# Kernel optimization log

Measured on AMD Instinct MI355X. Metric: run time of the kernel, lower is better.

The kernel has to match this reference:

```python
import jax, jax.numpy as jnp
import numpy as np

GROUPS = [1, 2, 2, 3]

def setup_inputs() -> dict:
    key = jax.random.key(0)
    ks = jax.random.split(key, 8)
    b, dim, h, w = 8, 256, 64, 64
    return {
        "x": jax.random.normal(ks[0], (b, dim, h, w), dtype=jnp.float32),
        "temperature": jnp.ones((4, 1, 1), dtype=jnp.float32),          # nn.Parameter(torch.ones(4,1,1))
        "w_qkv": jax.random.normal(ks[1], (3 * dim, dim)) * 0.02,        # Conv2d(dim,3dim,1,bias=False)
        "w_dw": jax.random.normal(ks[2], (3 * dim, 1, 3, 3)) * 0.1,      # depthwise 3x3, groups=3dim
        "w_proj": jax.random.normal(ks[3], (dim, dim)) * 0.02,           # Conv2d(dim,dim,1,bias=False)
        "w_gate": jax.random.normal(ks[4], (dim, dim)) * 0.02,           # Intra gatingConv (Conv1d k=1)
        "b_gate": jnp.zeros((dim,), dtype=jnp.float32),
        "w_down": jax.random.normal(ks[5], (dim // 2, dim)) * 0.02,      # Intra down
        "b_down": jnp.zeros((dim // 2,), dtype=jnp.float32),
        "w_up": jax.random.normal(ks[6], (dim, dim // 2)) * 0.02,        # Intra up
        "b_up": jnp.zeros((dim,), dtype=jnp.float32),
    }

def _l2norm(t):
    # torch F.normalize(dim=-1): x / max(||x||, 1e-12)
    return t / jnp.maximum(jnp.linalg.norm(t, axis=-1, keepdims=True), 1e-12)

def reference(x, temperature, w_qkv, w_dw, w_proj, w_gate, b_gate, w_down, b_down, w_up, b_up):
    b, c, h, w = x.shape
    L = h * w
    # qkv = dwconv3x3(conv1x1(x))
    qkv = jnp.einsum('bchw,oc->bohw', x, w_qkv)
    qkv = jax.lax.conv_general_dilated(qkv, w_dw, (1, 1), ((1, 1), (1, 1)),
                                       feature_group_count=3 * c,
                                       dimension_numbers=('NCHW', 'OIHW', 'NCHW'))
    q, k, v = jnp.split(qkv, 3, axis=1)
    q = q.reshape(b, c, L); k = k.reshape(b, c, L); v = v.reshape(b, c, L)
    # ReGroup: sort channels by mean activation (descending), split per ratio
    order = jnp.argsort(-q.mean(axis=2).mean(axis=0))
    qs, ks_, vs = q[:, order], k[:, order], v[:, order]
    total = sum(GROUPS)
    sizes = [int(r / total * c) for r in GROUPS]
    sizes[-1] += c - sum(sizes)
    outs, caches = [], []
    start = 0
    for i, g in enumerate(sizes):
        qg = qs[:, start:start + g]; kg = ks_[:, start:start + g]; vg = vs[:, start:start + g]
        start += g
        qn = _l2norm(qg); kn = _l2norm(kg)
        attn = jax.nn.softmax(jnp.einsum('bcl,bdl->bcd', qn, kn) * temperature[i], axis=-1)  # (b,Cg,Cg)
        caches.append(jax.lax.stop_gradient(qn + kn))  # q.detach()+k.detach()
        outs.append(jnp.einsum('bcd,bdl->bcl', attn, vg))
    # CalculateCurrentLayerCache: mean over L, channel-tile to c, bilinear 1x1->sxs == broadcast
    s = int(L ** 0.5 + 0.9999)
    accum = jnp.zeros((b, c), dtype=x.dtype)
    for tc, g in zip(caches, sizes):
        gm = tc.mean(axis=-1)                     # (b, Cg)
        rep = max(1, c // g)
        tiled = jnp.tile(gm, (1, rep))
        if tiled.shape[1] > c:
            tiled = tiled[:, :c]
        elif tiled.shape[1] < c:
            tiled = jnp.pad(tiled, ((0, 0), (0, c - tiled.shape[1])))
        accum = accum + tiled
    accum = accum / len(caches)
    qv_cache = 0.9 * jnp.broadcast_to(accum[:, :, None, None], (b, c, s, s))
    out_all = jnp.concatenate(outs, axis=1)       # (b, c, L)
    tmp_caches = jnp.concatenate(caches, axis=1)  # (b, c, L)
    # Intra_CacheModulation: gated = gelu(gateConv(z)) * z ; out = up(down(gated))
    z = tmp_caches + out_all
    gating = jax.nn.gelu(jnp.einsum('oc,bcl->bol', w_gate, z) + b_gate[None, :, None], approximate=False)
    gated = gating * z
    mid = jnp.einsum('oc,bcl->bol', w_down, gated) + b_down[None, :, None]
    intra = jnp.einsum('oc,bcl->bol', w_up, mid) + b_up[None, :, None]
    out_all = (intra + out_all).reshape(b, c, h, w)
    out_all = jnp.einsum('bchw,oc->bohw', out_all, w_proj)
    return (out_all, qv_cache)
```

## Files before the change

kernel.cpp:

```cpp
#include <hip/hip_runtime.h>
#include <hip/hip_fp16.h>
#include <math.h>

#define B 8
#define C 256
#define L 4096
#define OC3 768

typedef __attribute__((ext_vector_type(8))) short short8v;
typedef __attribute__((ext_vector_type(8))) unsigned short u16x8;
typedef __attribute__((ext_vector_type(4))) float f32x4;

__device__ __forceinline__ float gelu_exact(float x){
  return 0.5f * x * (1.0f + erff(x * 0.70710678118654752440f));
}
__device__ __forceinline__ float wave_sum(float v){
  #pragma unroll
  for (int off = 32; off > 0; off >>= 1) v += __shfl_down(v, off, 64);
  return v;
}
__device__ __forceinline__ unsigned short f16b(float f){
  return __half_as_ushort(__float2half_rn(f));
}
__device__ __forceinline__ float f16tof(unsigned short u){
  return __half2float(__ushort_as_half(u));
}
__device__ __forceinline__ unsigned int splitpackh(float v){
  unsigned short hi = f16b(v);
  float lof = v - f16tof(hi);
  unsigned short lo = f16b(lof);
  return (unsigned int)hi | ((unsigned int)lo << 16);
}
__device__ __forceinline__ void gl16(const unsigned short* g, unsigned short* l){
  __builtin_amdgcn_global_load_lds(
      (const __attribute__((address_space(1))) void*)g,
      (__attribute__((address_space(3))) void*)l, 16, 0, 0);
}

__global__ __launch_bounds__(256) void wsplit_kernel(
    const float* __restrict__ wqkv, const float* __restrict__ wgate,
    const float* __restrict__ wdown, const float* __restrict__ wup,
    const float* __restrict__ wproj,
    unsigned short* __restrict__ Wf16,
    unsigned short* __restrict__ PH, unsigned short* __restrict__ PLo)
{
  int idx = blockIdx.x * 256 + threadIdx.x;
  if (idx < 327680) {
    float s;
    if (idx < 196608)      s = wqkv[idx];
    else if (idx < 262144) s = wgate[idx - 196608];
    else if (idx < 294912) s = wdown[idx - 262144];
    else                   s = wup[idx - 294912];
    Wf16[idx] = f16b(s);
  } else {
    int j = idx - 327680;
    float wv = wproj[j];
    unsigned short hh = f16b(wv);
    PH[j]  = hh;
    PLo[j] = f16b(wv - f16tof(hh));
  }
}

__global__ __launch_bounds__(256) void splitx_kernel(const float* __restrict__ x,
    unsigned short* __restrict__ XThi, unsigned short* __restrict__ XTlo)
{
  __shared__ float st[64][68];
  const int b = blockIdx.z, c0 = blockIdx.y * 64, lb = blockIdx.x * 64;
  const int t = threadIdx.x;
  #pragma unroll
  for (int i = 0; i < 4; i++) {
    int row = (t >> 4) + i * 16;
    int col = (t & 15) * 4;
    float4 v = *(const float4*)&x[((size_t)b * C + c0 + row) * L + lb + col];
    st[row][col] = v.x; st[row][col+1] = v.y; st[row][col+2] = v.z; st[row][col+3] = v.w;
  }
  __syncthreads();
  const int l = t >> 2, cq = t & 3;
  u16x8 hv0, hv1, lv0, lv1;
  #pragma unroll
  for (int i = 0; i < 16; i++) {
    unsigned int p = splitpackh(st[cq * 16 + i][l]);
    if (i < 8) { hv0[i] = (unsigned short)(p & 0xFFFFu); lv0[i] = (unsigned short)(p >> 16); }
    else       { hv1[i-8] = (unsigned short)(p & 0xFFFFu); lv1[i-8] = (unsigned short)(p >> 16); }
  }
  size_t o = ((size_t)b * L + lb + l) * C + c0 + cq * 16;
  *(u16x8*)&XThi[o]     = hv0;
  *(u16x8*)&XThi[o + 8] = hv1;
  *(u16x8*)&XTlo[o]     = lv0;
  *(u16x8*)&XTlo[o + 8] = lv1;
}

template<int KTOT, int EPI, int MODE>
__global__ __launch_bounds__(256) void hgemm(
    const unsigned short* __restrict__ Ahi_g, const unsigned short* __restrict__ Alo_g,
    const unsigned short* __restrict__ Bw_g,
    float* __restrict__ outF,
    unsigned short* __restrict__ outH,
    int Ntot)
{
  __shared__ unsigned short SB[2][3][128 * 32];
  const int t  = threadIdx.x;
  const int lb = blockIdx.x * 128;
  const int o0 = blockIdx.y * 128;
  const int b  = blockIdx.z;
  const int w  = t >> 6, lane = t & 63;
  const int wm = w >> 1, wn = w & 1;
  const int ln = lane & 15, lg = lane >> 4;
  const int lrow  = lane >> 2;
  const int chunk = (lane & 3) ^ ((lane >> 4) & 3);
  const int slot  = lg ^ (ln >> 2);
  const bool twop = (blockIdx.y < 2);

  f32x4 z4 = {0.f, 0.f, 0.f, 0.f};
  f32x4 acc[4][4];
  #pragma unroll
  for (int i = 0; i < 4; i++)
    #pragma unroll
    for (int j = 0; j < 4; j++) acc[i][j] = z4;

  const size_t arow0 = (size_t)b * L + lb;
  constexpr int NKT = KTOT / 32;

  auto stage = [&](int kt, int cb) {
    const int k0 = kt * 32;
    #pragma unroll
    for (int i = 0; i < 2; i++) {
      const int rb = w * 32 + i * 16;
      const size_t ga = (arow0 + rb + lrow) * KTOT + k0 + chunk * 8;
      gl16(Ahi_g + ga, &SB[cb][0][rb * 32]);
      if (twop) gl16(Alo_g + ga, &SB[cb][1][rb * 32]);
      const size_t gb = (size_t)(o0 + rb + lrow) * KTOT + k0 + chunk * 8;
      gl16(Bw_g + gb, &SB[cb][2][rb * 32]);
    }
  };

  stage(0, 0);
  __syncthreads();
  int cur = 0;
  for (int kt = 0; kt < NKT; ++kt) {
    if (kt + 1 < NKT) stage(kt + 1, cur ^ 1);
    short8v bwf[4];
    #pragma unroll
    for (int nf = 0; nf < 4; nf++) {
      const int off = (wn * 64 + nf * 16 + ln) * 32 + slot * 8;
      bwf[nf] = *(const short8v*)&SB[cur][2][off];
    }
    #pragma unroll
    for (int mf = 0; mf < 4; mf++) {
      const int off = (wm * 64 + mf * 16 + ln) * 32 + slot * 8;
      const short8v ah = *(const short8v*)&SB[cur][0][off];
      #pragma unroll
      for (int nf = 0; nf < 4; nf++)
        acc[mf][nf] = __builtin_amdgcn_mfma_f32_16x16x32_f16(ah, bwf[nf], acc[mf][nf], 0, 0, 0);
      if (twop) {
        const short8v al = *(const short8v*)&SB[cur][1][off];
        #pragma unroll
        for (int nf = 0; nf < 4; nf++)
          acc[mf][nf] = __builtin_amdgcn_mfma_f32_16x16x32_f16(al, bwf[nf], acc[mf][nf], 0, 0, 0);
      }
    }
    __syncthreads();
    cur ^= 1;
  }
  #pragma unroll
  for (int mf = 0; mf < 4; mf++) {
    const int mbase = lb + wm * 64 + mf * 16 + lg * 4;
    #pragma unroll
    for (int nf = 0; nf < 4; nf++) {
      const int o = o0 + wn * 64 + nf * 16 + ln;
      if (o0 < 256) {
        float4 r;
        r.x = acc[mf][nf][0]; r.y = acc[mf][nf][1];
        r.z = acc[mf][nf][2]; r.w = acc[mf][nf][3];
        *(float4*)&outF[((size_t)b * 256 + o) * L + mbase] = r;
      } else {
        ushort4 r;
        r.x = f16b(acc[mf][nf][0]); r.y = f16b(acc[mf][nf][1]);
        r.z = f16b(acc[mf][nf][2]); r.w = f16b(acc[mf][nf][3]);
        *(ushort4*)&outH[((size_t)b * 512 + (o - 256)) * L + mbase] = r;
      }
    }
  }
}

__global__ __launch_bounds__(256, 2) void mlp_fused_kernel(
    const unsigned short* __restrict__ zT,
    const unsigned short* __restrict__ outT,
    const unsigned short* __restrict__ Wg,
    const unsigned short* __restrict__ Wd,
    const unsigned short* __restrict__ Wu,
    const unsigned short* __restrict__ WpH,
    const unsigned short* __restrict__ WpL,
    const float* __restrict__ bg, const float* __restrict__ bd, const float* __restrict__ bu,
    float* __restrict__ out0)
{
  __shared__ unsigned short zL[64 * 256];
  __shared__ unsigned short wL[2][64 * 128];
  __shared__ unsigned short mL[64 * 128];
  const int t = threadIdx.x;
  const int l0 = blockIdx.x * 64;
  const int b  = blockIdx.y;
  const int w = t >> 6, lane = t & 63;
  const int ln = lane & 15, lg = lane >> 4;

  {
    const int rIn = lane >> 5, ch = lane & 31;
    #pragma unroll
    for (int j = 0; j < 8; j++) {
      const int rowbase = w * 16 + j * 2;
      const int row = rowbase + rIn;
      const int sc = ch ^ (row & 7);
      gl16(zT + ((size_t)b * L + l0 + row) * 256 + sc * 8, &zL[rowbase * 256]);
    }
  }
  auto issueW = [&](int cb, const unsigned short* src, int rowstride) {
    const int rIn = lane >> 4, ch = lane & 15;
    #pragma unroll
    for (int j = 0; j < 4; j++) {
      const int rowbase = j * 16 + w * 4;
      const int row = rowbase + rIn;
      const int sc = ch ^ (row & 7);
      gl16(src + (size_t)row * rowstride + sc * 8, &wL[cb][rowbase * 128]);
    }
  };
  auto fragZ = [&](int row, int cc) -> short8v {
    return *(const short8v*)&zL[row * 256 + (cc ^ (row & 7)) * 8];
  };
  auto fragW = [&](int cb, int row, int cc) -> short8v {
    return *(const short8v*)&wL[cb][row * 128 + (cc ^ (row & 7)) * 8];
  };
  auto fragM = [&](int row, int cc) -> short8v {
    return *(const short8v*)&mL[row * 128 + (cc ^ (row & 7)) * 8];
  };
  auto gemmZt = [&](f32x4 (&acc)[4], int buf, int cbase) {
    #pragma unroll
    for (int ks = 0; ks < 4; ks++) {
      const short8v af = fragZ(w * 16 + ln, cbase + ks * 4 + lg);
      #pragma unroll
      for (int nf = 0; nf < 4; nf++) {
        const short8v bf = fragW(buf, nf * 16 + ln, ks * 4 + lg);
        acc[nf] = __builtin_amdgcn_mfma_f32_16x16x32_f16(af, bf, acc[nf], 0, 0, 0);
      }
    }
  };
  auto gemmMt = [&](f32x4 (&acc)[4], int buf) {
    #pragma unroll
    for (int ks = 0; ks < 4; ks++) {
      const short8v af = fragM(w * 16 + ln, ks * 4 + lg);
      #pragma unroll
      for (int nf = 0; nf < 4; nf++) {
        const short8v bf = fragW(buf, nf * 16 + ln, ks * 4 + lg);
        acc[nf] = __builtin_amdgcn_mfma_f32_16x16x32_f16(af, bf, acc[nf], 0, 0, 0);
      }
    }
  };

  const f32x4 zz = {0.f, 0.f, 0.f, 0.f};
  issueW(0, Wg, 256);
  __syncthreads();

  f32x4 aG[4][4];
  #pragma unroll
  for (int i = 0; i < 4; i++)
    #pragma unroll
    for (int j = 0; j < 4; j++) aG[i][j] = zz;
  issueW(1, Wg + 128,           256); gemmZt(aG[0], 0, 0);  __syncthreads();
  issueW(0, Wg + 64*256,        256); gemmZt(aG[0], 1, 16); __syncthreads();
  issueW(1, Wg + 64*256 + 128,  256); gemmZt(aG[1], 0, 0);  __syncthreads();
  issueW(0, Wg + 128*256,       256); gemmZt(aG[1], 1, 16); __syncthreads();
  issueW(1, Wg + 128*256 + 128, 256); gemmZt(aG[2], 0, 0);  __syncthreads();
  issueW(0, Wg + 192*256,       256); gemmZt(aG[2], 1, 16); __syncthreads();
  issueW(1, Wg + 192*256 + 128, 256); gemmZt(aG[3], 0, 0);  __syncthreads();
  issueW(0, Wd,                 256); gemmZt(aG[3], 1, 16); __syncthreads();
  #pragma unroll
  for (int oc = 0; oc < 4; oc++)
    #pragma unroll
    for (int nf = 0; nf < 4; nf++)
      #pragma unroll
      for (int r = 0; r < 4; r++) {
        const int l = w * 16 + lg * 4 + r;
        const int o = oc * 64 + nf * 16 + ln;
        const int a = l * 256 + (((o >> 3) ^ (l & 7)) << 3) + (o & 7);
        zL[a] = f16b(gelu_exact(aG[oc][nf][r] + bg[o]) * f16tof(zL[a]));
      }
  f32x4 aD[2][4];
  #pragma unroll
  for (int i = 0; i < 2; i++)
    #pragma unroll
    for (int j = 0; j < 4; j++) aD[i][j] = zz;
  issueW(1, Wd + 128,           256); gemmZt(aD[0], 0, 0);  __syncthreads();
  issueW(0, Wd + 64*256,        256); gemmZt(aD[0], 1, 16); __syncthreads();
  issueW(1, Wd + 64*256 + 128,  256); gemmZt(aD[1], 0, 0);  __syncthreads();
  issueW(0, Wu,                 128); gemmZt(aD[1], 1, 16); __syncthreads();
  #pragma unroll
  for (int oc = 0; oc < 2; oc++)
    #pragma unroll
    for (int nf = 0; nf < 4; nf++)
      #pragma unroll
      for (int r = 0; r < 4; r++) {
        const int l = w * 16 + lg * 4 + r;
        const int o = oc * 64 + nf * 16 + ln;
        mL[l * 128 + (((o >> 3) ^ (l & 7)) << 3) + (o & 7)] = f16b(aD[oc][nf][r] + bd[o]);
      }
  f32x4 aU[4][4];
  #pragma unroll
  for (int i = 0; i < 4; i++)
    #pragma unroll
    for (int j = 0; j < 4; j++) aU[i][j] = zz;
  issueW(1, Wu + 64*128,        128); gemmMt(aU[0], 0); __syncthreads();
  issueW(0, Wu + 128*128,       128); gemmMt(aU[1], 1); __syncthreads();
  issueW(1, Wu + 192*128,       128); gemmMt(aU[2], 0); __syncthreads();
  issueW(0, WpH,                256); gemmMt(aU[3], 1); __syncthreads();
  #pragma unroll
  for (int oc = 0; oc < 4; oc++)
    #pragma unroll
    for (int nf = 0; nf < 4; nf++)
      #pragma unroll
      for (int r = 0; r < 4; r++) {
        const int l = w * 16 + lg * 4 + r;
        const int o = oc * 64 + nf * 16 + ln;
        const float v = aU[oc][nf][r] + bu[o]
                      + f16tof(outT[((size_t)b * L + l0 + l) * 256 + o]);
        zL[l * 256 + (((o >> 3) ^ (l & 7)) << 3) + (o & 7)] = f16b(v);
      }
  f32x4 aP[4][4];
  #pragma unroll
  for (int i = 0; i < 4; i++)
    #pragma unroll
    for (int j = 0; j < 4; j++) aP[i][j] = zz;
  issueW(1, WpL,                256); gemmZt(aP[0], 0, 0);  __syncthreads();
  issueW(0, WpH + 128,          256); gemmZt(aP[0], 1, 0);  __syncthreads();
  issueW(1, WpL + 128,          256); gemmZt(aP[0], 0, 16); __syncthreads();
  issueW(0, WpH + 64*256,       256); gemmZt(aP[0], 1, 16); __syncthreads();
  issueW(1, WpL + 64*256,       256); gemmZt(aP[1], 0, 0);  __syncthreads();
  issueW(0, WpH + 64*256 + 128, 256); gemmZt(aP[1], 1, 0);  __syncthreads();
  issueW(1, WpL + 64*256 + 128, 256); gemmZt(aP[1], 0, 16); __syncthreads();
  issueW(0, WpH + 128*256,      256); gemmZt(aP[1], 1, 16); __syncthreads();
  issueW(1, WpL + 128*256,      256); gemmZt(aP[2], 0, 0);  __syncthreads();
  issueW(0, WpH + 128*256 + 128,256); gemmZt(aP[2], 1, 0);  __syncthreads();
  issueW(1, WpL + 128*256 + 128,256); gemmZt(aP[2], 0, 16); __syncthreads();
  issueW(0, WpH + 192*256,      256); gemmZt(aP[2], 1, 16); __syncthreads();
  issueW(1, WpL + 192*256,      256); gemmZt(aP[3], 0, 0);  __syncthreads();
  issueW(0, WpH + 192*256 + 128,256); gemmZt(aP[3], 1, 0);  __syncthreads();
  issueW(1, WpL + 192*256 + 128,256); gemmZt(aP[3], 0, 16); __syncthreads();
                                      gemmZt(aP[3], 1, 16);
  #pragma unroll
  for (int oc = 0; oc < 4; oc++)
    #pragma unroll
    for (int nf = 0; nf < 4; nf++) {
      const int o = oc * 64 + nf * 16 + ln;
      float4 r4;
      r4.x = aP[oc][nf][0]; r4.y = aP[oc][nf][1];
      r4.z = aP[oc][nf][2]; r4.w = aP[oc][nf][3];
      *(float4*)&out0[((size_t)b * 256 + o) * L + l0 + w * 16 + lg * 4] = r4;
    }
}

__global__ __launch_bounds__(256) void dwconv2_kernel(
    const float* __restrict__ inQ, const unsigned short* __restrict__ inKV,
    const float* __restrict__ wdw,
    unsigned short* __restrict__ qkF, unsigned short* __restrict__ vF,
    float* __restrict__ csum, float* __restrict__ csumsq)
{
  __shared__ float p[66][73];
  __shared__ float rs[4][2];
  const int ch = blockIdx.x;
  const int b  = blockIdx.y;
  const int t  = threadIdx.x;
  float wt[9];
  #pragma unroll
  for (int j = 0; j < 9; j++) wt[j] = wdw[ch * 9 + j];
  if (t < 66) { p[0][3 + t] = 0.f; p[65][3 + t] = 0.f; }
  if (t < 64) { p[1 + t][3] = 0.f; p[1 + t][68] = 0.f; }
  if (ch < 256) {
    const size_t base = ((size_t)b * 256 + ch) * L;
    #pragma unroll
    for (int i = 0; i < 4; i++) {
      int pix = (i * 256 + t) * 4;
      const float4 v = *reinterpret_cast<const float4*>(&inQ[base + pix]);
      int h = pix >> 6, ww = pix & 63;
      p[1+h][4+ww] = v.x; p[1+h][5+ww] = v.y; p[1+h][6+ww] = v.z; p[1+h][7+ww] = v.w;
    }
  } else {
    const size_t base = ((size_t)b * 512 + (ch - 256)) * L + t * 16;
    const u16x8 a0 = *(const u16x8*)&inKV[base];
    const u16x8 a1 = *(const u16x8*)&inKV[base + 8];
    const int h = t >> 2, w0 = (t & 3) * 16;
    #pragma unroll
    for (int j = 0; j < 8; j++) {
      p[1+h][4+w0+j]   = f16tof((unsigned short)a0[j]);
      p[1+h][12+w0+j]  = f16tof((unsigned short)a1[j]);
    }
  }
  __syncthreads();
  const int h  = t >> 2;
  const int w0 = (t & 3) * 16;
  float r0a[18], r1a[18], r2a[18];
  #pragma unroll
  for (int c = 0; c < 18; c++) {
    r0a[c] = p[h][w0 + 3 + c];
    r1a[c] = p[h + 1][w0 + 3 + c];
    r2a[c] = p[h + 2][w0 + 3 + c];
  }
  float res[16];
  float s = 0.f, s2 = 0.f;
  #pragma unroll
  for (int j = 0; j < 16; j++) {
    float acc;
    acc = r0a[j] * wt[0];
    acc = fmaf(r0a[j+1], wt[1], acc);
    acc = fmaf(r0a[j+2], wt[2], acc);
    acc = fmaf(r1a[j],   wt[3], acc);
    acc = fmaf(r1a[j+1], wt[4], acc);
    acc = fmaf(r1a[j+2], wt[5], acc);
    acc = fmaf(r2a[j],   wt[6], acc);
    acc = fmaf(r2a[j+1], wt[7], acc);
    acc = fmaf(r2a[j+2], wt[8], acc);
    res[j] = acc;
    s += acc;
    s2 = fmaf(acc, acc, s2);
  }
  u16x8 h0v, h1v;
  #pragma unroll
  for (int j = 0; j < 16; j++) {
    if (j < 8) h0v[j]   = f16b(res[j]);
    else       h1v[j-8] = f16b(res[j]);
  }
  if (ch < 512) {
    const size_t qi = ((size_t)b * 512 + ch) * L + t * 16;
    *(u16x8*)&qkF[qi]     = h0v;
    *(u16x8*)&qkF[qi + 8] = h1v;
    s = wave_sum(s); s2 = wave_sum(s2);
    const int lane = t & 63, wid = t >> 6;
    if (lane == 0) { rs[wid][0] = s; rs[wid][1] = s2; }
    __syncthreads();
    if (t == 0) {
      csum[b * 512 + ch]   = rs[0][0] + rs[1][0] + rs[2][0] + rs[3][0];
      csumsq[b * 512 + ch] = rs[0][1] + rs[1][1] + rs[2][1] + rs[3][1];
    }
  } else {
    const size_t vi = ((size_t)b * 256 + (ch - 512)) * L + t * 16;
    *(u16x8*)&vF[vi]     = h0v;
    *(u16x8*)&vF[vi + 8] = h1v;
  }
}

__global__ __launch_bounds__(256) void rankstats_kernel(
    const float* __restrict__ csum, const float* __restrict__ csumsq,
    int* __restrict__ order,
    float* __restrict__ sumq, float* __restrict__ sumk,
    float* __restrict__ invnq, float* __restrict__ invnk)
{
  const int c = threadIdx.x;
  float key = 0.f;
  #pragma unroll
  for (int b = 0; b < 8; b++) key += csum[b * 512 + c];
  __shared__ float keys[256];
  __shared__ int ordS[256];
  keys[c] = key;
  __syncthreads();
  int rank = 0;
  for (int j = 0; j < 256; j++) {
    float kj = keys[j];
    rank += (kj > key) || (kj == key && j < c);
  }
  order[rank] = c;
  ordS[rank] = c;
  __syncthreads();
  const int ch = ordS[c];
  #pragma unroll
  for (int b = 0; b < 8; b++) {
    sumq[b * 256 + c]  = csum[b * 512 + ch];
    invnq[b * 256 + c] = 1.0f / fmaxf(sqrtf(csumsq[b * 512 + ch]), 1e-12f);
    sumk[b * 256 + c]  = csum[b * 512 + 256 + ch];
    invnk[b * 256 + c] = 1.0f / fmaxf(sqrtf(csumsq[b * 512 + 256 + ch]), 1e-12f);
  }
}

__global__ __launch_bounds__(256) void vpack_kernel(
    const unsigned short* __restrict__ vF, const unsigned short* __restrict__ qkF,
    const int* __restrict__ order,
    const float* __restrict__ invnq, const float* __restrict__ invnk,
    unsigned short* __restrict__ vTS, unsigned short* __restrict__ zqT)
{
  __shared__ float vt[64][65];
  __shared__ float zt[64][65];
  __shared__ int   ordS[256];
  __shared__ float iqS[256], ikS[256];
  const int t = threadIdx.x, lb = blockIdx.x * 64, b = blockIdx.y;
  ordS[t] = order[t];
  iqS[t] = invnq[b * 256 + t];
  ikS[t] = invnk[b * 256 + t];
  __syncthreads();
  for (int cc = 0; cc < 4; cc++) {
    const int r0 = cc * 64;
    for (int i = t; i < 1024; i += 256) {
      const int row = i >> 4, q = i & 15;
      const int ch = ordS[r0 + row];
      const float iq = iqS[r0 + row], ik = ikS[r0 + row];
      const ushort4 v4 = *(const ushort4*)&vF[((size_t)b * 256 + ch) * L + lb + q * 4];
      vt[q*4+0][row] = f16tof(v4.x); vt[q*4+1][row] = f16tof(v4.y);
      vt[q*4+2][row] = f16tof(v4.z); vt[q*4+3][row] = f16tof(v4.w);
      const ushort4 q4 = *(const ushort4*)&qkF[((size_t)b * 512 + ch) * L + lb + q * 4];
      const ushort4 k4 = *(const ushort4*)&qkF[((size_t)b * 512 + 256 + ch) * L + lb + q * 4];
      zt[q*4+0][row] = f16tof(q4.x) * iq + f16tof(k4.x) * ik;
      zt[q*4+1][row] = f16tof(q4.y) * iq + f16tof(k4.y) * ik;
      zt[q*4+2][row] = f16tof(q4.z) * iq + f16tof(k4.z) * ik;
      zt[q*4+3][row] = f16tof(q4.w) * iq + f16tof(k4.w) * ik;
    }
    __syncthreads();
    const int l = t >> 2, qq = t & 3;
    const size_t ob = ((size_t)b * L + lb + l) * 256 + r0 + qq * 16;
    u16x8 vv[2], zz[2];
    #pragma unroll
    for (int j = 0; j < 16; j++) {
      vv[j>>3][j&7] = f16b(vt[l][qq*16 + j]);
      zz[j>>3][j&7] = f16b(zt[l][qq*16 + j]);
    }
    *(u16x8*)&vTS[ob]     = vv[0]; *(u16x8*)&vTS[ob + 8] = vv[1];
    *(u16x8*)&zqT[ob]     = zz[0]; *(u16x8*)&zqT[ob + 8] = zz[1];
    __syncthreads();
  }
}

template<int G, int GI, int START, int MB, int SPB>
__device__ void scores_body(const unsigned short* __restrict__ qkF,
    const int* __restrict__ order, float* __restrict__ Spart,
    unsigned short* Ah, unsigned short* Bh, int* ordS)
{
  constexpr int MR = (G - MB * 64 < 64) ? (G - MB * 64) : 64;
  constexpr int NF = G / 16;
  const int t = threadIdx.x, ks = blockIdx.x, b = blockIdx.y;
  const int w = t >> 6, lane = t & 63, ln = lane & 15, lg = lane >> 4;
  const int lrow  = lane >> 2;
  const int chunk = (lane & 3) ^ ((lane >> 4) & 3);
  const int slot  = lg ^ (ln >> 2);
  for (int i = t; i < G; i += 256) ordS[i] = order[START + i];
  __syncthreads();
  const int k0 = ks * 512;
  const bool act = (w * 16) < MR;
  f32x4 z4 = {0.f, 0.f, 0.f, 0.f};
  f32x4 acc[NF];
  #pragma unroll
  for (int i = 0; i < NF; i++) acc[i] = z4;

  auto stage = [&](int kc, int cb) {
    for (int i = w; i < MR / 16; i += 4) {
      const int rb = i * 16;
      const int ch = ordS[MB * 64 + rb + lrow];
      const size_t g = ((size_t)b * 512 + ch) * L + k0 + kc + chunk * 8;
      gl16(qkF + g, &Ah[cb * 2048 + rb * 32]);
    }
    for (int i = w; i < G / 16; i += 4) {
      const int rb = i * 16;
      const int ch = 256 + ordS[rb + lrow];
      const size_t g = ((size_t)b * 512 + ch) * L + k0 + kc + chunk * 8;
      gl16(qkF + g, &Bh[cb * 3072 + rb * 32]);
    }
  };

  stage(0, 0);
  __syncthreads();
  int cur = 0;
  for (int kc = 0; kc < 512; kc += 32) {
    if (kc + 32 < 512) stage(kc + 32, cur ^ 1);
    if (act) {
      const int aoff = cur * 2048 + (w * 16 + ln) * 32 + slot * 8;
      const short8v ah = *(const short8v*)&Ah[aoff];
      #pragma unroll
      for (int nf = 0; nf < NF; nf++) {
        const int boff = cur * 3072 + (nf * 16 + ln) * 32 + slot * 8;
        const short8v bh = *(const short8v*)&Bh[boff];
        acc[nf] = __builtin_amdgcn_mfma_f32_16x16x32_f16(ah, bh, acc[nf], 0, 0, 0);
      }
    }
    __syncthreads();
    cur ^= 1;
  }
  if (act) {
    float* dst = Spart + (size_t)b * 147456 + SPB + ks * G * G;
    #pragma unroll
    for (int nf = 0; nf < NF; nf++) {
      const int d = nf * 16 + ln;
      #pragma unroll
      for (int r = 0; r < 4; r++) {
        const int m = MB * 64 + w * 16 + lg * 4 + r;
        dst[m * G + d] = acc[nf][r];
      }
    }
  }
}

__global__ __launch_bounds__(256) void scores_kernel(const unsigned short* __restrict__ qkF,
    const int* __restrict__ order, float* __restrict__ Spart)
{
  __shared__ unsigned short Ah[2 * 64 * 32];
  __shared__ unsigned short Bh[2 * 96 * 32];
  __shared__ int ordS[96];
  switch (blockIdx.z) {
    case 0:  scores_body<32, 0, 0,   0, 0    >(qkF, order, Spart, Ah, Bh, ordS); break;
    case 1:  scores_body<64, 1, 32,  0, 8192 >(qkF, order, Spart, Ah, Bh, ordS); break;
    case 2:  scores_body<64, 2, 96,  0, 40960>(qkF, order, Spart, Ah, Bh, ordS); break;
    case 3:  scores_body<96, 3, 160, 0, 73728>(qkF, order, Spart, Ah, Bh, ordS); break;
    default: scores_body<96, 3, 160, 1, 73728>(qkF, order, Spart, Ah, Bh, ordS); break;
  }
}

template<int G, int GI, int START, int SPB, int AOFF>
__device__ void softmax_body(const float* __restrict__ Spart, const float* __restrict__ invnq,
    const float* __restrict__ invnk, const float* __restrict__ temperature,
    unsigned short* __restrict__ attnP, float* Sm)
{
  constexpr int RQ = G / 4;
  const int t = threadIdx.x;
  const int b = blockIdx.x;
  const int r0 = blockIdx.z * RQ;
  const float temp = temperature[GI];
  for (int idx = t; idx < RQ * G; idx += 256) {
    const int rl = idx / G, d = idx - rl * G;
    const int gidx = (r0 + rl) * G + d;
    float s = 0.f;
    #pragma unroll
    for (int ks = 0; ks < 8; ks++)
      s += Spart[(size_t)b * 147456 + SPB + ks * G * G + gidx];
    Sm[idx] = s * invnq[b * 256 + START + r0 + rl] * invnk[b * 256 + START + d] * temp;
  }
  __syncthreads();
  const int wv = t >> 6, lane = t & 63;
  for (int r = wv; r < RQ; r += 4) {
    const float v0 = (lane < G) ? Sm[r * G + lane] : -INFINITY;
    const float v1 = (64 + lane < G) ? Sm[r * G + 64 + lane] : -INFINITY;
    float m = fmaxf(v0, v1);
    #pragma unroll
    for (int off = 32; off > 0; off >>= 1) m = fmaxf(m, __shfl_xor(m, off, 64));
    const float e0 = (lane < G) ? expf(v0 - m) : 0.f;
    const float e1 = (64 + lane < G) ? expf(v1 - m) : 0.f;
    float s = e0 + e1;
    #pragma unroll
    for (int off = 32; off > 0; off >>= 1) s += __shfl_xor(s, off, 64);
    const float inv = 1.0f / s;
    const size_t base = (size_t)b * 18432 + AOFF + (size_t)(r0 + r) * G;
    if (lane < G)      attnP[base + lane]      = f16b(e0 * inv);
    if (64 + lane < G) attnP[base + 64 + lane] = f16b(e1 * inv);
  }
}

__global__ __launch_bounds__(256) void softmax_kernel(const float* __restrict__ Spart,
    const float* __restrict__ invnq, const float* __restrict__ invnk,
    const float* __restrict__ temperature, unsigned short* __restrict__ attnP)
{
  extern __shared__ float smem[];
  switch (blockIdx.y) {
    case 0:  softmax_body<32, 0, 0,   0,     0   >(Spart, invnq, invnk, temperature, attnP, smem); break;
    case 1:  softmax_body<64, 1, 32,  8192,  1024>(Spart, invnq, invnk, temperature, attnP, smem); break;
    case 2:  softmax_body<64, 2, 96,  40960, 5120>(Spart, invnq, invnk, temperature, attnP, smem); break;
    default: softmax_body<96, 3, 160, 73728, 9216>(Spart, invnq, invnk, temperature, attnP, smem); break;
  }
}

template<int G, int GI, int START, int AOFF>
__device__ void pv_body(
    const unsigned short* __restrict__ vTS, const unsigned short* __restrict__ attnP,
    const unsigned short* __restrict__ zqT,
    unsigned short* __restrict__ outT, unsigned short* __restrict__ zT,
    unsigned short* Ah, unsigned short* Bh)
{
  constexpr int NF = G / 16;
  const int t = threadIdx.x, b = blockIdx.y, l0 = blockIdx.x * 128;
  const int w = t >> 6, lane = t & 63, ln = lane & 15, lg = lane >> 4;
  const int lrow  = lane >> 2;
  const int chunk = (lane & 3) ^ ((lane >> 4) & 3);
  const int slot  = lg ^ (ln >> 2);
  f32x4 z4 = {0.f, 0.f, 0.f, 0.f};
  f32x4 acc[2][NF];
  #pragma unroll
  for (int i = 0; i < 2; i++)
    #pragma unroll
    for (int j = 0; j < NF; j++) acc[i][j] = z4;
  for (int kc = 0; kc < G; kc += 32) {
    #pragma unroll
    for (int i = 0; i < 2; i++) {
      const int rb = w * 32 + i * 16;
      const size_t g = ((size_t)b * L + l0 + rb + lrow) * 256 + START + kc + chunk * 8;
      gl16(vTS + g, &Ah[rb * 32]);
    }
    for (int i = w; i < G / 16; i += 4) {
      const int rb = i * 16;
      const size_t g = (size_t)b * 18432 + AOFF + (size_t)(rb + lrow) * G + kc + chunk * 8;
      gl16(attnP + g, &Bh[rb * 32]);
    }
    __syncthreads();
    short8v bhf[NF];
    #pragma unroll
    for (int nf = 0; nf < NF; nf++)
      bhf[nf] = *(const short8v*)&Bh[(nf * 16 + ln) * 32 + slot * 8];
    #pragma unroll
    for (int mi = 0; mi < 2; mi++) {
      const int aoff = ((w * 2 + mi) * 16 + ln) * 32 + slot * 8;
      const short8v ah = *(const short8v*)&Ah[aoff];
      #pragma unroll
      for (int nf = 0; nf < NF; nf++)
        acc[mi][nf] = __builtin_amdgcn_mfma_f32_16x16x32_f16(ah, bhf[nf], acc[mi][nf], 0, 0, 0);
    }
    __syncthreads();
  }
  #pragma unroll
  for (int mi = 0; mi < 2; mi++) {
    const int lbase = l0 + (w * 2 + mi) * 16 + lg * 4;
    #pragma unroll
    for (int nf = 0; nf < NF; nf++) {
      const int col = START + nf * 16 + ln;
      #pragma unroll
      for (int r = 0; r < 4; r++) {
        const size_t idx = ((size_t)b * L + lbase + r) * 256 + col;
        const float v = acc[mi][nf][r];
        outT[idx] = f16b(v);
        zT[idx]   = f16b(v + f16tof(zqT[idx]));
      }
    }
  }
}

__global__ __launch_bounds__(256) void pv_kernel(
    const unsigned short* __restrict__ vTS, const unsigned short* __restrict__ attnP,
    const unsigned short* __restrict__ zqT,
    unsigned short* __restrict__ outT, unsigned short* __restrict__ zT)
{
  __shared__ unsigned short Ah[128 * 32];
  __shared__ unsigned short Bh[96 * 32];
  switch (blockIdx.z) {
    case 0:  pv_body<32, 0, 0,   0   >(vTS, attnP, zqT, outT, zT, Ah, Bh); break;
    case 1:  pv_body<64, 1, 32,  1024>(vTS, attnP, zqT, outT, zT, Ah, Bh); break;
    case 2:  pv_body<64, 2, 96,  5120>(vTS, attnP, zqT, outT, zT, Ah, Bh); break;
    default: pv_body<96, 3, 160, 9216>(vTS, attnP, zqT, outT, zT, Ah, Bh); break;
  }
}

__global__ __launch_bounds__(256) void qv_kernel(const float* __restrict__ sumq,
    const float* __restrict__ sumk, const float* __restrict__ invnq,
    const float* __restrict__ invnk, float* __restrict__ out2)
{
  const int b = blockIdx.x >> 8, r = blockIdx.x & 255;
  float val = 0.f;
  {
    const int idx = b * 256 + 0 + (r & 31);
    val += fmaf(sumq[idx], invnq[idx], sumk[idx] * invnk[idx]);
  }
  {
    const int idx = b * 256 + 32 + (r & 63);
    val += fmaf(sumq[idx], invnq[idx], sumk[idx] * invnk[idx]);
  }
  {
    const int idx = b * 256 + 96 + (r & 63);
    val += fmaf(sumq[idx], invnq[idx], sumk[idx] * invnk[idx]);
  }
  if (r < 192) {
    const int rm = (r < 96) ? r : r - 96;
    const int idx = b * 256 + 160 + rm;
    val += fmaf(sumq[idx], invnq[idx], sumk[idx] * invnk[idx]);
  }
  val *= (1.0f / 4096.f) * 0.25f * 0.9f;
  const float4 o = {val, val, val, val};
  float4* dst = reinterpret_cast<float4*>(out2 + ((size_t)b * C + r) * L);
  for (int i = threadIdx.x; i < 1024; i += 256) dst[i] = o;
}

extern "C" void kernel_launch(void* const* d_in, const int* in_sizes, int n_in,
                              void* d_out, int out_size, void* d_ws, size_t ws_size,
                              hipStream_t stream)
{
  const float* x           = (const float*)d_in[0];
  const float* temperature = (const float*)d_in[1];
  const float* w_qkv       = (const float*)d_in[2];
  const float* w_dw        = (const float*)d_in[3];
  const float* w_proj      = (const float*)d_in[4];
  const float* w_gate      = (const float*)d_in[5];
  const float* b_gate      = (const float*)d_in[6];
  const float* w_down      = (const float*)d_in[7];
  const float* b_down      = (const float*)d_in[8];
  const float* w_up        = (const float*)d_in[9];
  const float* b_up        = (const float*)d_in[10];

  if (ws_size < 202548224ULL) return;

  char* ws = (char*)d_ws;
  float*          qkvQ    = (float*)(ws);
  unsigned short* kvF     = (unsigned short*)(ws + 33554432);
  unsigned short* vTS     = (unsigned short*)(ws);
  unsigned short* zqT     = (unsigned short*)(ws + 16777216);
  float*          Spart   = (float*)(ws + 33554432);
  unsigned short* attnP   = (unsigned short*)(ws + 38797312);
  unsigned short* XThi    = (unsigned short*)(ws + 100663296);
  unsigned short* XTlo    = (unsigned short*)(ws + 117440512);
  unsigned short* qkF     = (unsigned short*)(ws + 100663296);
  unsigned short* vF      = (unsigned short*)(ws + 134217728);
  unsigned short* outT    = (unsigned short*)(ws + 150994944);
  unsigned short* zT      = (unsigned short*)(ws + 167772160);
  unsigned short* Wf16   = (unsigned short*)(ws + 201326592);
  unsigned short* WprojH = (unsigned short*)(ws + 201981952);
  unsigned short* WprojL = (unsigned short*)(ws + 202113024);
  float* csum   = (float*)(ws + 202244096);
  float* csumsq = (float*)(ws + 202260480);
  float* sumq   = (float*)(ws + 202276864);
  float* sumk   = (float*)(ws + 202285056);
  float* invnq  = (float*)(ws + 202293248);
  float* invnk  = (float*)(ws + 202301440);
  int*   order  = (int*)(ws + 202309632);

  float* out_all = (float*)d_out;
  float* qv_out  = out_all + (size_t)B * C * L;

  wsplit_kernel<<<1536, 256, 0, stream>>>(w_qkv, w_gate, w_down, w_up, w_proj,
                                          Wf16, WprojH, WprojL);
  splitx_kernel<<<dim3(64, 4, 8), 256, 0, stream>>>(x, XThi, XTlo);
  hgemm<256, 6, 2><<<dim3(32, 6, 8), 256, 0, stream>>>(
      XThi, XTlo, Wf16, qkvQ, kvF, 768);
  dwconv2_kernel<<<dim3(768, 8), 256, 0, stream>>>(qkvQ, kvF, w_dw, qkF, vF, csum, csumsq);
  rankstats_kernel<<<1, 256, 0, stream>>>(csum, csumsq, order, sumq, sumk, invnq, invnk);
  vpack_kernel<<<dim3(64, 8), 256, 0, stream>>>(vF, qkF, order, invnq, invnk, vTS, zqT);
  scores_kernel<<<dim3(8, 8, 5), 256, 0, stream>>>(qkF, order, Spart);
  softmax_kernel<<<dim3(8, 4, 4), 256, 9216, stream>>>(Spart, invnq, invnk, temperature, attnP);
  pv_kernel<<<dim3(32, 8, 4), 256, 0, stream>>>(vTS, attnP, zqT, outT, zT);
  mlp_fused_kernel<<<dim3(64, 8), 256, 0, stream>>>(
      zT, outT, Wf16 + 196608, Wf16 + 262144, Wf16 + 294912, WprojH, WprojL,
      b_gate, b_down, b_up, out_all);
  qv_kernel<<<2048, 256, 0, stream>>>(sumq, sumk, invnq, invnk, qv_out);
}
```

Before: 206.8 us.

## Restructure fused MLP kernel into a 4-buffer, depth-2 weight prefetch pipeline

The fused gate/down/up/proj kernel now runs as one unrolled 64-stage loop over 64x64 weight tiles. A descriptor function maps each stage to its slice of a single combined weight buffer. Tiles rotate through four LDS buffers, are prefetched two stages ahead, and are synchronised with explicit vmcnt waits and raw s_barrier, replacing a full __syncthreads per 64x128 step. The down-projection intermediate now reuses the z LDS region, which lowers LDS use and could raise occupancy. This assumes the projection hi/lo weights sit at fixed offsets inside Wf16 and adds fine-grained synchronisation that is fragile around the phase transitions.

```diff
diff --git a/kernel.cpp b/kernel.cpp
--- a/kernel.cpp
+++ b/kernel.cpp
@@ -183,20 +183,29 @@
   }
 }
 
+struct SDesc { unsigned int woff; int stride; int acc; int cbase; int isM; };
+__device__ __forceinline__ SDesc sdesc(int s){
+  if (s < 16) { int rg = s >> 2, kc = s & 3;
+    SDesc d = {196608u + (unsigned)(rg * 64 * 256 + kc * 64), 256, rg, kc * 8, 0}; return d; }
+  if (s < 24) { int i = s - 16; int rg = i >> 2, kc = i & 3;
+    SDesc d = {262144u + (unsigned)(rg * 64 * 256 + kc * 64), 256, rg, kc * 8, 0}; return d; }
+  if (s < 32) { int i = s - 24; int rg = i >> 1, kc = i & 1;
+    SDesc d = {294912u + (unsigned)(rg * 64 * 128 + kc * 64), 128, rg, kc * 8, 1}; return d; }
+  int i = s - 32; int rg = i >> 3, pl = (i >> 2) & 1, kc = i & 3;
+  SDesc d = {(pl ? 393216u : 327680u) + (unsigned)(rg * 64 * 256 + kc * 64), 256, rg, kc * 8, 0};
+  return d;
+}
+
 __global__ __launch_bounds__(256, 2) void mlp_fused_kernel(
     const unsigned short* __restrict__ zT,
     const unsigned short* __restrict__ outT,
-    const unsigned short* __restrict__ Wg,
-    const unsigned short* __restrict__ Wd,
-    const unsigned short* __restrict__ Wu,
-    const unsigned short* __restrict__ WpH,
-    const unsigned short* __restrict__ WpL,
+    const unsigned short* __restrict__ Wmega,
     const float* __restrict__ bg, const float* __restrict__ bd, const float* __restrict__ bu,
     float* __restrict__ out0)
 {
   __shared__ unsigned short zL[64 * 256];
-  __shared__ unsigned short wL[2][64 * 128];
-  __shared__ unsigned short mL[64 * 128];
+  __shared__ unsigned short wL[4][64 * 64];
+  unsigned short* mL = zL;
   const int t = threadIdx.x;
   const int l0 = blockIdx.x * 64;
   const int b  = blockIdx.y;
@@ -213,145 +222,132 @@
       gl16(zT + ((size_t)b * L + l0 + row) * 256 + sc * 8, &zL[rowbase * 256]);
     }
   }
-  auto issueW = [&](int cb, const unsigned short* src, int rowstride) {
-    const int rIn = lane >> 4, ch = lane & 15;
-    #pragma unroll
-    for (int j = 0; j < 4; j++) {
-      const int rowbase = j * 16 + w * 4;
+  auto issueW = [&](int cb, unsigned int woff, int stride) {
+    const int rIn = lane >> 3, ch = lane & 7;
+    #pragma unroll
+    for (int j = 0; j < 2; j++) {
+      const int rowbase = w * 16 + j * 8;
       const int row = rowbase + rIn;
       const int sc = ch ^ (row & 7);
-      gl16(src + (size_t)row * rowstride + sc * 8, &wL[cb][rowbase * 128]);
+      gl16(Wmega + (size_t)woff + (size_t)row * stride + sc * 8, &wL[cb][rowbase * 64]);
     }
   };
   auto fragZ = [&](int row, int cc) -> short8v {
     return *(const short8v*)&zL[row * 256 + (cc ^ (row & 7)) * 8];
   };
   auto fragW = [&](int cb, int row, int cc) -> short8v {
-    return *(const short8v*)&wL[cb][row * 128 + (cc ^ (row & 7)) * 8];
+    return *(const short8v*)&wL[cb][row * 64 + (cc ^ (row & 7)) * 8];
   };
   auto fragM = [&](int row, int cc) -> short8v {
     return *(const short8v*)&mL[row * 128 + (cc ^ (row & 7)) * 8];
   };
-  auto gemmZt = [&](f32x4 (&acc)[4], int buf, int cbase) {
-    #pragma unroll
-    for (int ks = 0; ks < 4; ks++) {
-      const short8v af = fragZ(w * 16 + ln, cbase + ks * 4 + lg);
-      #pragma unroll
-      for (int nf = 0; nf < 4; nf++) {
-        const short8v bf = fragW(buf, nf * 16 + ln, ks * 4 + lg);
-        acc[nf] = __builtin_amdgcn_mfma_f32_16x16x32_f16(af, bf, acc[nf], 0, 0, 0);
+
+  const f32x4 zz = {0.f, 0.f, 0.f, 0.f};
+  f32x4 acc[4][4];
+  #pragma unroll
+  for (int i = 0; i < 4; i++)
+    #pragma unroll
+    for (int j = 0; j < 4; j++) acc[i][j] = zz;
+
+  { SDesc d = sdesc(0); issueW(0, d.woff, d.stride); }
+  { SDesc d = sdesc(1); issueW(1, d.woff, d.stride); }
+
+  #pragma unroll
+  for (int s = 0; s < 64; ++s) {
+    if (s + 2 < 64) { SDesc d2 = sdesc(s + 2); issueW((s + 2) & 3, d2.woff, d2.stride); }
+    if (s <= 61)      asm volatile("s_waitcnt vmcnt(4)" ::: "memory");
+    else if (s == 62) asm volatile("s_waitcnt vmcnt(2)" ::: "memory");
+    else              asm volatile("s_waitcnt vmcnt(0)" ::: "memory");
+    __builtin_amdgcn_sched_barrier(0);
+    __builtin_amdgcn_s_barrier();
+    __builtin_amdgcn_sched_barrier(0);
+    {
+      SDesc d = sdesc(s);
+      const int buf = s & 3;
+      if (d.isM) {
+        #pragma unroll
+        for (int ks = 0; ks < 2; ks++) {
+          const short8v af = fragM(w * 16 + ln, d.cbase + ks * 4 + lg);
+          #pragma unroll
+          for (int nf = 0; nf < 4; nf++) {
+            const short8v bf = fragW(buf, nf * 16 + ln, ks * 4 + lg);
+            acc[d.acc][nf] = __builtin_amdgcn_mfma_f32_16x16x32_f16(af, bf, acc[d.acc][nf], 0, 0, 0);
+          }
+        }
+      } else {
+        #pragma unroll
+        for (int ks = 0; ks < 2; ks++) {
+          const short8v af = fragZ(w * 16 + ln, d.cbase + ks * 4 + lg);
+          #pragma unroll
+          for (int nf = 0; nf < 4; nf++) {
+            const short8v bf = fragW(buf, nf * 16 + ln, ks * 4 + lg);
+            acc[d.acc][nf] = __builtin_amdgcn_mfma_f32_16x16x32_f16(af, bf, acc[d.acc][nf], 0, 0, 0);
+          }
+        }
       }
     }
-  };
-  auto gemmMt = [&](f32x4 (&acc)[4], int buf) {
-    #pragma unroll
-    for (int ks = 0; ks < 4; ks++) {
-      const short8v af = fragM(w * 16 + ln, ks * 4 + lg);
-      #pragma unroll
-      for (int nf = 0; nf < 4; nf++) {
-        const short8v bf = fragW(buf, nf * 16 + ln, ks * 4 + lg);
-        acc[nf] = __builtin_amdgcn_mfma_f32_16x16x32_f16(af, bf, acc[nf], 0, 0, 0);
-      }
-    }
-  };
-
-  const f32x4 zz = {0.f, 0.f, 0.f, 0.f};
-  issueW(0, Wg, 256);
-  __syncthreads();
-
-  f32x4 aG[4][4];
-  #pragma unroll
-  for (int i = 0; i < 4; i++)
-    #pragma unroll
-    for (int j = 0; j < 4; j++) aG[i][j] = zz;
-  issueW(1, Wg + 128,           256); gemmZt(aG[0], 0, 0);  __syncthreads();
-  issueW(0, Wg + 64*256,        256); gemmZt(aG[0], 1, 16); __syncthreads();
-  issueW(1, Wg + 64*256 + 128,  256); gemmZt(aG[1], 0, 0);  __syncthreads();
-  issueW(0, Wg + 128*256,       256); gemmZt(aG[1], 1, 16); __syncthreads();
-  issueW(1, Wg + 128*256 + 128, 256); gemmZt(aG[2], 0, 0);  __syncthreads();
-  issueW(0, Wg + 192*256,       256); gemmZt(aG[2], 1, 16); __syncthreads();
-  issueW(1, Wg + 192*256 + 128, 256); gemmZt(aG[3], 0, 0);  __syncthreads();
-  issueW(0, Wd,                 256); gemmZt(aG[3], 1, 16); __syncthreads();
-  #pragma unroll
-  for (int oc = 0; oc < 4; oc++)
-    #pragma unroll
-    for (int nf = 0; nf < 4; nf++)
-      #pragma unroll
-      for (int r = 0; r < 4; r++) {
-        const int l = w * 16 + lg * 4 + r;
-        const int o = oc * 64 + nf * 16 + ln;
-        const int a = l * 256 + (((o >> 3) ^ (l & 7)) << 3) + (o & 7);
-        zL[a] = f16b(gelu_exact(aG[oc][nf][r] + bg[o]) * f16tof(zL[a]));
-      }
-  f32x4 aD[2][4];
-  #pragma unroll
-  for (int i = 0; i < 2; i++)
-    #pragma unroll
-    for (int j = 0; j < 4; j++) aD[i][j] = zz;
-  issueW(1, Wd + 128,           256); gemmZt(aD[0], 0, 0);  __syncthreads();
-  issueW(0, Wd + 64*256,        256); gemmZt(aD[0], 1, 16); __syncthreads();
-  issueW(1, Wd + 64*256 + 128,  256); gemmZt(aD[1], 0, 0);  __syncthreads();
-  issueW(0, Wu,                 128); gemmZt(aD[1], 1, 16); __syncthreads();
-  #pragma unroll
-  for (int oc = 0; oc < 2; oc++)
-    #pragma unroll
-    for (int nf = 0; nf < 4; nf++)
-      #pragma unroll
-      for (int r = 0; r < 4; r++) {
-        const int l = w * 16 + lg * 4 + r;
-        const int o = oc * 64 + nf * 16 + ln;
-        mL[l * 128 + (((o >> 3) ^ (l & 7)) << 3) + (o & 7)] = f16b(aD[oc][nf][r] + bd[o]);
-      }
-  f32x4 aU[4][4];
-  #pragma unroll
-  for (int i = 0; i < 4; i++)
-    #pragma unroll
-    for (int j = 0; j < 4; j++) aU[i][j] = zz;
-  issueW(1, Wu + 64*128,        128); gemmMt(aU[0], 0); __syncthreads();
-  issueW(0, Wu + 128*128,       128); gemmMt(aU[1], 1); __syncthreads();
-  issueW(1, Wu + 192*128,       128); gemmMt(aU[2], 0); __syncthreads();
-  issueW(0, WpH,                256); gemmMt(aU[3], 1); __syncthreads();
-  #pragma unroll
-  for (int oc = 0; oc < 4; oc++)
-    #pragma unroll
-    for (int nf = 0; nf < 4; nf++)
-      #pragma unroll
-      for (int r = 0; r < 4; r++) {
-        const int l = w * 16 + lg * 4 + r;
-        const int o = oc * 64 + nf * 16 + ln;
-        const float v = aU[oc][nf][r] + bu[o]
-                      + f16tof(outT[((size_t)b * L + l0 + l) * 256 + o]);
-        zL[l * 256 + (((o >> 3) ^ (l & 7)) << 3) + (o & 7)] = f16b(v);
-      }
-  f32x4 aP[4][4];
-  #pragma unroll
-  for (int i = 0; i < 4; i++)
-    #pragma unroll
-    for (int j = 0; j < 4; j++) aP[i][j] = zz;
-  issueW(1, WpL,                256); gemmZt(aP[0], 0, 0);  __syncthreads();
-  issueW(0, WpH + 128,          256); gemmZt(aP[0], 1, 0);  __syncthreads();
-  issueW(1, WpL + 128,          256); gemmZt(aP[0], 0, 16); __syncthreads();
-  issueW(0, WpH + 64*256,       256); gemmZt(aP[0], 1, 16); __syncthreads();
-  issueW(1, WpL + 64*256,       256); gemmZt(aP[1], 0, 0);  __syncthreads();
-  issueW(0, WpH + 64*256 + 128, 256); gemmZt(aP[1], 1, 0);  __syncthreads();
-  issueW(1, WpL + 64*256 + 128, 256); gemmZt(aP[1], 0, 16); __syncthreads();
-  issueW(0, WpH + 128*256,      256); gemmZt(aP[1], 1, 16); __syncthreads();
-  issueW(1, WpL + 128*256,      256); gemmZt(aP[2], 0, 0);  __syncthreads();
-  issueW(0, WpH + 128*256 + 128,256); gemmZt(aP[2], 1, 0);  __syncthreads();
-  issueW(1, WpL + 128*256 + 128,256); gemmZt(aP[2], 0, 16); __syncthreads();
-  issueW(0, WpH + 192*256,      256); gemmZt(aP[2], 1, 16); __syncthreads();
-  issueW(1, WpL + 192*256,      256); gemmZt(aP[3], 0, 0);  __syncthreads();
-  issueW(0, WpH + 192*256 + 128,256); gemmZt(aP[3], 1, 0);  __syncthreads();
-  issueW(1, WpL + 192*256 + 128,256); gemmZt(aP[3], 0, 16); __syncthreads();
-                                      gemmZt(aP[3], 1, 16);
+    if (s == 15) {
+      #pragma unroll
+      for (int oc = 0; oc < 4; oc++)
+        #pragma unroll
+        for (int nf = 0; nf < 4; nf++)
+          #pragma unroll
+          for (int r = 0; r < 4; r++) {
+            const int l = w * 16 + lg * 4 + r;
+            const int o = oc * 64 + nf * 16 + ln;
+            const int a = l * 256 + (((o >> 3) ^ (l & 7)) << 3) + (o & 7);
+            zL[a] = f16b(gelu_exact(acc[oc][nf][r] + bg[o]) * f16tof(zL[a]));
+          }
+      #pragma unroll
+      for (int i = 0; i < 4; i++)
+        #pragma unroll
+        for (int j = 0; j < 4; j++) acc[i][j] = zz;
+    }
+    if (s == 23) {
+      __syncthreads();
+      #pragma unroll
+      for (int oc = 0; oc < 2; oc++)
+        #pragma unroll
+        for (int nf = 0; nf < 4; nf++)
+          #pragma unroll
+          for (int r = 0; r < 4; r++) {
+            const int l = w * 16 + lg * 4 + r;
+            const int o = oc * 64 + nf * 16 + ln;
+            mL[l * 128 + (((o >> 3) ^ (l & 7)) << 3) + (o & 7)] = f16b(acc[oc][nf][r] + bd[o]);
+          }
+      #pragma unroll
+      for (int i = 0; i < 4; i++)
+        #pragma unroll
+        for (int j = 0; j < 4; j++) acc[i][j] = zz;
+    }
+    if (s == 31) {
+      __syncthreads();
+      #pragma unroll
+      for (int oc = 0; oc < 4; oc++)
+        #pragma unroll
+        for (int nf = 0; nf < 4; nf++)
+          #pragma unroll
+          for (int r = 0; r < 4; r++) {
+            const int l = w * 16 + lg * 4 + r;
+            const int o = oc * 64 + nf * 16 + ln;
+            const float v = acc[oc][nf][r] + bu[o]
+                          + f16tof(outT[((size_t)b * L + l0 + l) * 256 + o]);
+            zL[l * 256 + (((o >> 3) ^ (l & 7)) << 3) + (o & 7)] = f16b(v);
+          }
+      #pragma unroll
+      for (int i = 0; i < 4; i++)
+        #pragma unroll
+        for (int j = 0; j < 4; j++) acc[i][j] = zz;
+    }
+  }
   #pragma unroll
   for (int oc = 0; oc < 4; oc++)
     #pragma unroll
     for (int nf = 0; nf < 4; nf++) {
       const int o = oc * 64 + nf * 16 + ln;
       float4 r4;
-      r4.x = aP[oc][nf][0]; r4.y = aP[oc][nf][1];
-      r4.z = aP[oc][nf][2]; r4.w = aP[oc][nf][3];
+      r4.x = acc[oc][nf][0]; r4.y = acc[oc][nf][1];
+      r4.z = acc[oc][nf][2]; r4.w = acc[oc][nf][3];
       *(float4*)&out0[((size_t)b * 256 + o) * L + l0 + w * 16 + lg * 4] = r4;
     }
 }
@@ -822,7 +818,6 @@
   softmax_kernel<<<dim3(8, 4, 4), 256, 9216, stream>>>(Spart, invnq, invnk, temperature, attnP);
   pv_kernel<<<dim3(32, 8, 4), 256, 0, stream>>>(vTS, attnP, zqT, outT, zT);
   mlp_fused_kernel<<<dim3(64, 8), 256, 0, stream>>>(
-      zT, outT, Wf16 + 196608, Wf16 + 262144, Wf16 + 294912, WprojH, WprojL,
-      b_gate, b_down, b_up, out_all);
+      zT, outT, Wf16, b_gate, b_down, b_up, out_all);
   qv_kernel<<<2048, 256, 0, stream>>>(sumq, sumk, invnq, invnk, qv_out);
 }
```

Result: slower. 333.1 us (+61.1%).

## Triple-buffer MLP weight tiles with partial vmcnt waits and single barriers

Applied to the files above, without the earlier changes.

Weight tiles in the fused MLP kernel move from a double buffer to a three-slot ring. Each stage now waits only until at most four global-to-LDS loads are outstanding (s_waitcnt vmcnt(4)) before a raw s_barrier, so the next tile's load overlaps the current MFMA stage instead of fully draining every step. The down-projection intermediate mL is aliased onto zL to pay for the extra buffer and keep LDS use roughly unchanged. The hand-coded wait counts depend on the number of loads issueW emits per thread, and the zL aliasing depends on the added __syncthreads placement, so any mismatch is a correctness risk.

```diff
diff --git a/kernel.cpp b/kernel.cpp
--- a/kernel.cpp
+++ b/kernel.cpp
@@ -36,6 +36,12 @@
       (const __attribute__((address_space(1))) void*)g,
       (__attribute__((address_space(3))) void*)l, 16, 0, 0);
 }
+#define WAITB4 do { asm volatile("s_waitcnt vmcnt(4)" ::: "memory"); \
+  __builtin_amdgcn_sched_barrier(0); __builtin_amdgcn_s_barrier(); \
+  __builtin_amdgcn_sched_barrier(0); } while(0)
+#define WAITB0 do { asm volatile("s_waitcnt vmcnt(0)" ::: "memory"); \
+  __builtin_amdgcn_sched_barrier(0); __builtin_amdgcn_s_barrier(); \
+  __builtin_amdgcn_sched_barrier(0); } while(0)
 
 __global__ __launch_bounds__(256) void wsplit_kernel(
     const float* __restrict__ wqkv, const float* __restrict__ wgate,
@@ -195,8 +201,8 @@
     float* __restrict__ out0)
 {
   __shared__ unsigned short zL[64 * 256];
-  __shared__ unsigned short wL[2][64 * 128];
-  __shared__ unsigned short mL[64 * 128];
+  __shared__ unsigned short wL[3][64 * 128];
+  unsigned short* mL = zL;
   const int t = threadIdx.x;
   const int l0 = blockIdx.x * 64;
   const int b  = blockIdx.y;
@@ -257,21 +263,20 @@
 
   const f32x4 zz = {0.f, 0.f, 0.f, 0.f};
   issueW(0, Wg, 256);
-  __syncthreads();
 
   f32x4 aG[4][4];
   #pragma unroll
   for (int i = 0; i < 4; i++)
     #pragma unroll
     for (int j = 0; j < 4; j++) aG[i][j] = zz;
-  issueW(1, Wg + 128,           256); gemmZt(aG[0], 0, 0);  __syncthreads();
-  issueW(0, Wg + 64*256,        256); gemmZt(aG[0], 1, 16); __syncthreads();
-  issueW(1, Wg + 64*256 + 128,  256); gemmZt(aG[1], 0, 0);  __syncthreads();
-  issueW(0, Wg + 128*256,       256); gemmZt(aG[1], 1, 16); __syncthreads();
-  issueW(1, Wg + 128*256 + 128, 256); gemmZt(aG[2], 0, 0);  __syncthreads();
-  issueW(0, Wg + 192*256,       256); gemmZt(aG[2], 1, 16); __syncthreads();
-  issueW(1, Wg + 192*256 + 128, 256); gemmZt(aG[3], 0, 0);  __syncthreads();
-  issueW(0, Wd,                 256); gemmZt(aG[3], 1, 16); __syncthreads();
+  issueW(1, Wg + 128,           256); WAITB4; gemmZt(aG[0], 0, 0);
+  issueW(2, Wg + 64*256,        256); WAITB4; gemmZt(aG[0], 1, 16);
+  issueW(0, Wg + 64*256 + 128,  256); WAITB4; gemmZt(aG[1], 2, 0);
+  issueW(1, Wg + 128*256,       256); WAITB4; gemmZt(aG[1], 0, 16);
+  issueW(2, Wg + 128*256 + 128, 256); WAITB4; gemmZt(aG[2], 1, 0);
+  issueW(0, Wg + 192*256,       256); WAITB4; gemmZt(aG[2], 2, 16);
+  issueW(1, Wg + 192*256 + 128, 256); WAITB4; gemmZt(aG[3], 0, 0);
+  issueW(2, Wd,                 256); WAITB4; gemmZt(aG[3], 1, 16);
   #pragma unroll
   for (int oc = 0; oc < 4; oc++)
     #pragma unroll
@@ -288,10 +293,11 @@
   for (int i = 0; i < 2; i++)
     #pragma unroll
     for (int j = 0; j < 4; j++) aD[i][j] = zz;
-  issueW(1, Wd + 128,           256); gemmZt(aD[0], 0, 0);  __syncthreads();
-  issueW(0, Wd + 64*256,        256); gemmZt(aD[0], 1, 16); __syncthreads();
-  issueW(1, Wd + 64*256 + 128,  256); gemmZt(aD[1], 0, 0);  __syncthreads();
-  issueW(0, Wu,                 128); gemmZt(aD[1], 1, 16); __syncthreads();
+  issueW(0, Wd + 128,           256); WAITB4; gemmZt(aD[0], 2, 0);
+  issueW(1, Wd + 64*256,        256); WAITB4; gemmZt(aD[0], 0, 16);
+  issueW(2, Wd + 64*256 + 128,  256); WAITB4; gemmZt(aD[1], 1, 0);
+  issueW(0, Wu,                 128); WAITB4; gemmZt(aD[1], 2, 16);
+  __syncthreads();
   #pragma unroll
   for (int oc = 0; oc < 2; oc++)
     #pragma unroll
@@ -307,10 +313,11 @@
   for (int i = 0; i < 4; i++)
     #pragma unroll
     for (int j = 0; j < 4; j++) aU[i][j] = zz;
-  issueW(1, Wu + 64*128,        128); gemmMt(aU[0], 0); __syncthreads();
-  issueW(0, Wu + 128*128,       128); gemmMt(aU[1], 1); __syncthreads();
-  issueW(1, Wu + 192*128,       128); gemmMt(aU[2], 0); __syncthreads();
-  issueW(0, WpH,                256); gemmMt(aU[3], 1); __syncthreads();
+  issueW(1, Wu + 64*128,        128); WAITB4; gemmMt(aU[0], 0);
+  issueW(2, Wu + 128*128,       128); WAITB4; gemmMt(aU[1], 1);
+  issueW(0, Wu + 192*128,       128); WAITB4; gemmMt(aU[2], 2);
+  issueW(1, WpH,                256); WAITB4; gemmMt(aU[3], 0);
+  __syncthreads();
   #pragma unroll
   for (int oc = 0; oc < 4; oc++)
     #pragma unroll
@@ -328,22 +335,22 @@
   for (int i = 0; i < 4; i++)
     #pragma unroll
     for (int j = 0; j < 4; j++) aP[i][j] = zz;
-  issueW(1, WpL,                256); gemmZt(aP[0], 0, 0);  __syncthreads();
-  issueW(0, WpH + 128,          256); gemmZt(aP[0], 1, 0);  __syncthreads();
-  issueW(1, WpL + 128,          256); gemmZt(aP[0], 0, 16); __syncthreads();
-  issueW(0, WpH + 64*256,       256); gemmZt(aP[0], 1, 16); __syncthreads();
-  issueW(1, WpL + 64*256,       256); gemmZt(aP[1], 0, 0);  __syncthreads();
-  issueW(0, WpH + 64*256 + 128, 256); gemmZt(aP[1], 1, 0);  __syncthreads();
-  issueW(1, WpL + 64*256 + 128, 256); gemmZt(aP[1], 0, 16); __syncthreads();
-  issueW(0, WpH + 128*256,      256); gemmZt(aP[1], 1, 16); __syncthreads();
-  issueW(1, WpL + 128*256,      256); gemmZt(aP[2], 0, 0);  __syncthreads();
-  issueW(0, WpH + 128*256 + 128,256); gemmZt(aP[2], 1, 0);  __syncthreads();
-  issueW(1, WpL + 128*256 + 128,256); gemmZt(aP[2], 0, 16); __syncthreads();
-  issueW(0, WpH + 192*256,      256); gemmZt(aP[2], 1, 16); __syncthreads();
-  issueW(1, WpL + 192*256,      256); gemmZt(aP[3], 0, 0);  __syncthreads();
-  issueW(0, WpH + 192*256 + 128,256); gemmZt(aP[3], 1, 0);  __syncthreads();
-  issueW(1, WpL + 192*256 + 128,256); gemmZt(aP[3], 0, 16); __syncthreads();
-                                      gemmZt(aP[3], 1, 16);
+  issueW(2, WpL,                256); WAITB4; gemmZt(aP[0], 1, 0);
+  issueW(0, WpH + 128,          256); WAITB4; gemmZt(aP[0], 2, 0);
+  issueW(1, WpL + 128,          256); WAITB4; gemmZt(aP[0], 0, 16);
+  issueW(2, WpH + 64*256,       256); WAITB4; gemmZt(aP[0], 1, 16);
+  issueW(0, WpL + 64*256,       256); WAITB4; gemmZt(aP[1], 2, 0);
+  issueW(1, WpH + 64*256 + 128, 256); WAITB4; gemmZt(aP[1], 0, 0);
+  issueW(2, WpL + 64*256 + 128, 256); WAITB4; gemmZt(aP[1], 1, 16);
+  issueW(0, WpH + 128*256,      256); WAITB4; gemmZt(aP[1], 2, 16);
+  issueW(1, WpL + 128*256,      256); WAITB4; gemmZt(aP[2], 0, 0);
+  issueW(2, WpH + 128*256 + 128,256); WAITB4; gemmZt(aP[2], 1, 0);
+  issueW(0, WpL + 128*256 + 128,256); WAITB4; gemmZt(aP[2], 2, 16);
+  issueW(1, WpH + 192*256,      256); WAITB4; gemmZt(aP[2], 0, 16);
+  issueW(2, WpL + 192*256,      256); WAITB4; gemmZt(aP[3], 1, 0);
+  issueW(0, WpH + 192*256 + 128,256); WAITB4; gemmZt(aP[3], 2, 0);
+  issueW(1, WpL + 192*256 + 128,256); WAITB4; gemmZt(aP[3], 0, 16);
+                                      WAITB0; gemmZt(aP[3], 1, 16);
   #pragma unroll
   for (int oc = 0; oc < 4; oc++)
     #pragma unroll
```

Measured after the change: 201.7 us. -2.5%, faster.
